# Kernel tuning notes

Measured on AMD Instinct MI355X. Metric: run time of the kernel, lower is better.

Reference implementation:

```python
import jax, jax.numpy as jnp
import numpy as np

E, N, D_IN, D_EMB, H = 4096, 4096, 256, 64, 8
HD = D_EMB * H
N_ETYPES, N_NTYPES = 4, 2
SCALE = D_EMB ** 0.5
EPS = 1e-5


def _layernorm(x, g, b):
    mu = jnp.mean(x, axis=-1, keepdims=True)
    var = jnp.var(x, axis=-1, keepdims=True)
    return (x - mu) / jnp.sqrt(var + EPS) * g + b


def setup_inputs() -> dict:
    key = jax.random.key(0)
    ks = jax.random.split(key, 14)
    s_in = 1.0 / np.sqrt(D_IN)
    s_cat = 1.0 / np.sqrt(HD + D_IN)
    return {
        "hyperedge_features": jax.random.normal(ks[0], (E, D_IN), jnp.float32),
        "node_features": jax.random.normal(ks[1], (N, D_IN), jnp.float32),
        "incidence_matrix": jax.random.randint(ks[2], (N, E), 0, 2, jnp.int32),
        "node_types": jax.random.randint(ks[3], (N,), 0, N_NTYPES, jnp.int32),
        "hyperedge_types": jax.random.randint(ks[4], (E,), 0, N_ETYPES, jnp.int32),
        # per-type expert weights (no bias in torch Linears)
        "Wq": jax.random.uniform(ks[5], (N_ETYPES, D_IN, HD), jnp.float32, -s_in, s_in),
        "Wk": jax.random.uniform(ks[6], (N_NTYPES, D_IN, HD), jnp.float32, -s_in, s_in),
        "Wv": jax.random.uniform(ks[7], (N_NTYPES, D_IN, HD), jnp.float32, -s_in, s_in),
        "Wo": jax.random.uniform(ks[8], (HD + D_IN, D_IN), jnp.float32, -s_cat, s_cat),
        "bo": jax.random.uniform(ks[9], (D_IN,), jnp.float32, -s_cat, s_cat),
        "gamma_e": jnp.ones((D_IN,), jnp.float32),
        "beta_e": jnp.zeros((D_IN,), jnp.float32),
        "gamma_n": jnp.ones((D_IN,), jnp.float32),
        "beta_n": jnp.zeros((D_IN,), jnp.float32),
    }


def reference(hyperedge_features, node_features, incidence_matrix, node_types,
              hyperedge_types, Wq, Wk, Wv, Wo, bo, gamma_e, beta_e, gamma_n, beta_n):
    he = _layernorm(hyperedge_features, gamma_e, beta_e)   # [E, D_IN]
    nf = _layernorm(node_features, gamma_n, beta_n)        # [N, D_IN]

    # type-conditional projections: compute all experts, gather per row
    q = jnp.einsum('ed,tdk->tek', he, Wq)[hyperedge_types, jnp.arange(E)]  # [E, HD]
    k = jnp.einsum('nd,tdk->tnk', nf, Wk)[node_types, jnp.arange(N)]      # [N, HD]
    v = jnp.einsum('nd,tdk->tnk', nf, Wv)[node_types, jnp.arange(N)]      # [N, HD]

    q = q.reshape(E, H, D_EMB).transpose(1, 0, 2)  # [H, E, D]
    k = k.reshape(N, H, D_EMB).transpose(1, 0, 2)  # [H, N, D]
    v = v.reshape(N, H, D_EMB).transpose(1, 0, 2)  # [H, N, D]

    scores = jnp.einsum('hed,hnd->hen', q, k) / SCALE        # [H, E, N]
    mask = incidence_matrix.T[None]                           # [1, E, N]
    scores = jnp.where(mask == 0, -jnp.inf, scores)
    weights = jax.nn.softmax(scores, axis=-1)                 # dropout in eval mode => identity

    out = jnp.einsum('hen,hnd->hed', weights, v)              # [H, E, D]
    out = out.transpose(1, 0, 2).reshape(E, HD)               # [E, HD]
    out = jax.nn.silu(out)

    final = jnp.concatenate([he, out], axis=-1) @ Wo + bo     # [E, D_IN]
    return final, scores
```

## Files before the change

kernel.cpp:

```cpp
#include <hip/hip_runtime.h>
#include <math.h>

#define E 4096
#define NN 4096
#define DIN 256
#define DEMB 64
#define NH 8
#define HD 512
#define EPS 1e-5f

typedef __bf16 bf16x8 __attribute__((ext_vector_type(8)));
typedef float f32x4 __attribute__((ext_vector_type(4)));

union FRS { uint4 u; bf16x8 b; unsigned short s[8]; };
union H4  { ushort4 u; unsigned short s[4]; };

#define MFMA __builtin_amdgcn_mfma_f32_16x16x32_bf16

__device__ __forceinline__ void splitf(float f, unsigned short& hs, unsigned short& ls) {
    unsigned u = __float_as_uint(f);
    hs = (unsigned short)(u >> 16);
    float rem = f - __uint_as_float(u & 0xffff0000u);
    ls = (unsigned short)(__float_as_uint(rem) >> 16);
}

__global__ void zero_counts(int* counts) {
    if (threadIdx.x < 8) counts[threadIdx.x] = 0;
}

__global__ void bucket_kernel(const int* __restrict__ et, const int* __restrict__ nt,
                              int* counts, int* ie, int* in_) {
    int i = blockIdx.x * 256 + threadIdx.x;
    if (i < E) {
        int t = et[i];
        int p = atomicAdd(&counts[t], 1);
        ie[t * E + p] = i;
    } else {
        int j = i - E;
        int t = nt[j];
        int p = atomicAdd(&counts[4 + t], 1);
        in_[t * NN + p] = j;
    }
}

__global__ __launch_bounds__(256) void incbits_kernel(const int* __restrict__ inc,
                                                      unsigned long long* __restrict__ ib) {
    int n = blockIdx.x;
    int l = threadIdx.x & 63, w = threadIdx.x >> 6;
    const int* row = inc + (size_t)n * E;
#pragma unroll
    for (int i = 0; i < 16; i++) {
        int word = i * 4 + w;
        unsigned long long b = __ballot(row[word * 64 + l] != 0);
        if (l == 0) ib[(size_t)n * 64 + word] = b;
    }
}

__global__ void bit_transpose(const unsigned long long* __restrict__ ib,
                              unsigned long long* __restrict__ it) {
    int nw = blockIdx.x, ew = blockIdx.y;
    int j = threadIdx.x;
    unsigned long long wv = ib[(size_t)(nw * 64 + j) * 64 + ew];
    unsigned long long mine = 0;
    for (int t2 = 0; t2 < 64; t2++) {
        unsigned long long b = __ballot((int)((wv >> t2) & 1ull));
        if (t2 == j) mine = b;
    }
    it[(size_t)(ew * 64 + j) * 64 + nw] = mine;
}

__device__ __forceinline__ float block_reduce_sum(float v, float* sm) {
    __syncthreads();
#pragma unroll
    for (int o = 32; o > 0; o >>= 1) v += __shfl_down(v, o, 64);
    int w = threadIdx.x >> 6, lane = threadIdx.x & 63;
    if (lane == 0) sm[w] = v;
    __syncthreads();
    return sm[0] + sm[1] + sm[2] + sm[3];
}

__global__ __launch_bounds__(256) void ln_kernel(const float* __restrict__ ef, const float* __restrict__ nf_in,
                          const float* __restrict__ ge, const float* __restrict__ be,
                          const float* __restrict__ gn, const float* __restrict__ bn,
                          float* __restrict__ he, float* __restrict__ nfo) {
    int row = blockIdx.x;
    const float* src; float* dst; const float* g; const float* b;
    if (row < E) { src = ef + (size_t)row * DIN; dst = he + (size_t)row * DIN; g = ge; b = be; }
    else { int r = row - E; src = nf_in + (size_t)r * DIN; dst = nfo + (size_t)r * DIN; g = gn; b = bn; }
    __shared__ float sm[4];
    int t = threadIdx.x;
    float x = src[t];
    float mu = block_reduce_sum(x, sm) * (1.f / DIN);
    float d = x - mu;
    float var = block_reduce_sum(d * d, sm) * (1.f / DIN);
    float rstd = rsqrtf(var + EPS);
    dst[t] = d * rstd * g[t] + b[t];
}

__global__ __launch_bounds__(256) void wconv(const float* __restrict__ src,
        char* __restrict__ dst, int Ktot, int Ctot) {
    int cb = blockIdx.x, kb = blockIdx.y, z = blockIdx.z;
    int CB = Ctot >> 6, KB = Ktot >> 6;
    const float* S = src + (size_t)z * Ktot * Ctot + (size_t)(kb * 64) * Ctot + cb * 64;
    char* D = dst + (((size_t)((z * CB + cb) * KB + kb)) << 14);
    __shared__ float Ls[64][68];
    int tid = threadIdx.x;
    int k = tid >> 2, cq = (tid & 3) * 16;
#pragma unroll
    for (int j = 0; j < 4; j++)
        *(float4*)&Ls[k][cq + j * 4] = *(const float4*)&S[(size_t)k * Ctot + cq + j * 4];
    __syncthreads();
    int c = tid >> 2, kq = (tid & 3) * 16;
    int sw = (c & 7) << 4;
#pragma unroll
    for (int grp = 0; grp < 4; grp++) {
        int k0 = kq + grp * 4;
        H4 hi, lo;
#pragma unroll
        for (int i = 0; i < 4; i++) splitf(Ls[k0 + i][c], hi.s[i], lo.s[i]);
        int off = (c * 128 + k0 * 2) ^ sw;
        *(ushort4*)(D + off) = hi.u;
        *(ushort4*)(D + 8192 + off) = lo.u;
    }
}

__global__ __launch_bounds__(256) void proj_mfma(const float* __restrict__ X,
        const char* __restrict__ wimg, const int* __restrict__ idx,
        const int* __restrict__ counts, int idxStride, int matBase,
        float* __restrict__ out) {
    int t = blockIdx.z;
    int cnt = counts[t];
    int r0 = blockIdx.y * 64;
    if (r0 >= cnt) return;
    int cb = blockIdx.x;
    const int* ib = idx + (size_t)t * idxStride;
    int tid = threadIdx.x;
    int w = tid >> 6, l = tid & 63, g = l >> 4, q = l & 15;
    __shared__ __align__(16) char XW[32768];
    int sm = tid >> 2, skq = (tid & 3) * 16;
    int srow = (r0 + sm < cnt) ? ib[r0 + sm] : -1;
    const int swz = (q & 7) << 4;
    const int sswz = (sm & 7) << 4;
    f32x4 acc[4] = {};
    const char* wtb = wimg + (((size_t)((matBase + t) * 8 + cb) * 4) << 14);
    for (int kb = 0; kb < 4; kb++) {
        __syncthreads();
#pragma unroll
        for (int c4 = 0; c4 < 4; c4++) {
            int gk = kb * 64 + skq + c4 * 4;
            float4 xv = (srow >= 0) ? *(const float4*)&X[(size_t)srow * DIN + gk]
                                    : make_float4(0.f, 0.f, 0.f, 0.f);
            float xf[4] = {xv.x, xv.y, xv.z, xv.w};
            H4 hi, lo;
#pragma unroll
            for (int i = 0; i < 4; i++) splitf(xf[i], hi.s[i], lo.s[i]);
            int off = (sm * 128 + (skq + c4 * 4) * 2) ^ sswz;
            *(ushort4*)(XW + off) = hi.u;
            *(ushort4*)(XW + 8192 + off) = lo.u;
        }
        const char* wt = wtb + ((size_t)kb << 14);
#pragma unroll
        for (int i = 0; i < 4; i++)
            *(uint4*)(XW + 16384 + i * 4096 + tid * 16) = *(const uint4*)(wt + i * 4096 + tid * 16);
        __syncthreads();
        FRS bh[2], bl[2];
#pragma unroll
        for (int ks = 0; ks < 2; ks++) {
            int boff = (w * 16 + q) * 128 + ((ks * 64 + g * 16) ^ swz);
            bh[ks].u = *(const uint4*)(XW + 16384 + boff);
            bl[ks].u = *(const uint4*)(XW + 24576 + boff);
        }
#pragma unroll
        for (int mt = 0; mt < 4; mt++) {
#pragma unroll
            for (int ks = 0; ks < 2; ks++) {
                int aoff = (mt * 16 + q) * 128 + ((ks * 64 + g * 16) ^ swz);
                FRS ah, al;
                ah.u = *(const uint4*)(XW + aoff);
                al.u = *(const uint4*)(XW + 8192 + aoff);
                acc[mt] = MFMA(ah.b, bh[ks].b, acc[mt], 0, 0, 0);
                acc[mt] = MFMA(ah.b, bl[ks].b, acc[mt], 0, 0, 0);
                acc[mt] = MFMA(al.b, bh[ks].b, acc[mt], 0, 0, 0);
            }
        }
    }
#pragma unroll
    for (int mt = 0; mt < 4; mt++)
#pragma unroll
        for (int r = 0; r < 4; r++) {
            int rg = r0 + mt * 16 + 4 * g + r;
            if (rg < cnt)
                out[(size_t)ib[rg] * HD + cb * 64 + w * 16 + q] = acc[mt][r];
        }
}

__global__ __launch_bounds__(256) void kconv(const float* __restrict__ kbuf,
                                             char* __restrict__ stage) {
    int gid = blockIdx.x * 256 + threadIdx.x;
    int d8 = gid & 7, hh = (gid >> 3) & 7;
    int n = gid >> 6;
    const float* src = kbuf + (size_t)n * HD + hh * 64 + d8 * 8;
    float4 a = *(const float4*)src, b = *(const float4*)(src + 4);
    float fv[8] = {a.x, a.y, a.z, a.w, b.x, b.y, b.z, b.w};
    FRS hi, lo;
#pragma unroll
    for (int j = 0; j < 8; j++) splitf(fv[j], hi.s[j], lo.s[j]);
    char* blk = stage + ((size_t)(hh * 64 + (n >> 6)) << 15);
    int nl = n & 63;
    int off = (nl * 128 + d8 * 16) ^ ((nl & 7) << 4);
    *(uint4*)(blk + off) = hi.u;
    *(uint4*)(blk + 8192 + off) = lo.u;
}

__global__ __launch_bounds__(256) void vconv(const float* __restrict__ vbuf,
                                             char* __restrict__ stage) {
    int tt = blockIdx.x, hh = blockIdx.y;
    __shared__ float Ls[64][68];
    int tid = threadIdx.x;
    int n = tid >> 2, q4 = (tid & 3) * 16;
#pragma unroll
    for (int j = 0; j < 4; j++)
        *(float4*)&Ls[n][q4 + j * 4] =
            *(const float4*)&vbuf[(size_t)(tt * 64 + n) * HD + hh * DEMB + q4 + j * 4];
    __syncthreads();
    char* blk = stage + ((size_t)(hh * 64 + tt) << 15);
    int d = tid >> 2, ng = tid & 3;
    int dsw = (d & 7) << 4;
#pragma unroll
    for (int sub = 0; sub < 4; sub++) {
        int n0 = ng * 16 + sub * 4;
        H4 hi, lo;
#pragma unroll
        for (int i = 0; i < 4; i++) splitf(Ls[n0 + i][d], hi.s[i], lo.s[i]);
        int s0 = ((n0 >> 5) << 5) + (((n0 >> 2) & 3) << 3) + (((n0 >> 4) & 1) << 2);
        int off = (d * 128 + s0 * 2) ^ dsw;
        *(ushort4*)(blk + 16384 + off) = hi.u;
        *(ushort4*)(blk + 24576 + off) = lo.u;
    }
}

__global__ __launch_bounds__(256, 2) void attn_mfma(
    const float* __restrict__ qb, const char* __restrict__ kvstage,
    const unsigned long long* __restrict__ incT,
    float* __restrict__ sc, float* __restrict__ pO,
    float* __restrict__ pm, float* __restrict__ plv)
{
    const int bx = blockIdx.x, h = blockIdx.y, nz = blockIdx.z;
    const int tid = threadIdx.x;
    const int w = tid >> 6, l = tid & 63;
    const int g = l >> 4, q = l & 15;
    const int e_wave = bx * 128 + w * 32;
    const int T0 = nz * 32;

    __shared__ __align__(16) char kv[2][32768];

    FRS qh[2][2], ql[2][2];
#pragma unroll
    for (int et = 0; et < 2; et++) {
        const float* qrow = qb + (size_t)(e_wave + et * 16 + q) * HD + h * DEMB;
#pragma unroll
        for (int ks = 0; ks < 2; ks++) {
            float4 A = *(const float4*)(qrow + ks * 32 + g * 8);
            float4 B = *(const float4*)(qrow + ks * 32 + g * 8 + 4);
            float fv[8] = {A.x, A.y, A.z, A.w, B.x, B.y, B.z, B.w};
            FRS hh, ll;
#pragma unroll
            for (int j = 0; j < 8; j++) splitf(fv[j], hh.s[j], ll.s[j]);
            qh[et][ks] = hh; ql[et][ks] = ll;
        }
    }

    uint4 streg[8];
    {
        const char* gs = kvstage + ((size_t)(h * 64 + T0) << 15);
#pragma unroll
        for (int i = 0; i < 8; i++) streg[i] = *(const uint4*)(gs + i * 4096 + tid * 16);
#pragma unroll
        for (int i = 0; i < 8; i++) *(uint4*)(&kv[0][i * 4096 + tid * 16]) = streg[i];
    }
    __syncthreads();

    f32x4 oacc[2][4];
#pragma unroll
    for (int et = 0; et < 2; et++)
#pragma unroll
        for (int dt = 0; dt < 4; dt++) oacc[et][dt] = (f32x4){0.f, 0.f, 0.f, 0.f};
    float mrow[2] = {-INFINITY, -INFINITY}, lrow[2] = {0.f, 0.f};
    const int swz = (q & 7) << 4;

    for (int tt = 0; tt < 32; tt++) {
        const int t = T0 + tt;
        const int cur = tt & 1;
        if (tt < 31) {
            const char* gs = kvstage + ((size_t)(h * 64 + t + 1) << 15);
#pragma unroll
            for (int i = 0; i < 8; i++) streg[i] = *(const uint4*)(gs + i * 4096 + tid * 16);
        }
        f32x4 sacc[2][4];
#pragma unroll
        for (int et = 0; et < 2; et++)
#pragma unroll
            for (int nt = 0; nt < 4; nt++) sacc[et][nt] = (f32x4){0.f, 0.f, 0.f, 0.f};
        const char* Kh = &kv[cur][0];
        const char* Kl = &kv[cur][8192];
#pragma unroll
        for (int ks = 0; ks < 2; ks++) {
#pragma unroll
            for (int nt = 0; nt < 4; nt++) {
                int off = (nt * 16 + q) * 128 + ((ks * 64 + g * 16) ^ swz);
                FRS ah, al;
                ah.u = *(const uint4*)(Kh + off);
                al.u = *(const uint4*)(Kl + off);
#pragma unroll
                for (int et = 0; et < 2; et++) {
                    sacc[et][nt] = MFMA(ah.b, qh[et][ks].b, sacc[et][nt], 0, 0, 0);
                    sacc[et][nt] = MFMA(ah.b, ql[et][ks].b, sacc[et][nt], 0, 0, 0);
                    sacc[et][nt] = MFMA(al.b, qh[et][ks].b, sacc[et][nt], 0, 0, 0);
                }
            }
        }
        float alpha_s[2];
#pragma unroll
        for (int et = 0; et < 2; et++) {
            int e = e_wave + et * 16 + q;
            unsigned long long mw = incT[(size_t)e * 64 + t];
            float rmax = -INFINITY;
#pragma unroll
            for (int nt = 0; nt < 4; nt++) {
                unsigned nib = (unsigned)(mw >> (nt * 16 + g * 4)) & 0xfu;
                f32x4 s4 = sacc[et][nt];
                f32x4 w4;
#pragma unroll
                for (int r = 0; r < 4; r++) {
                    float v = s4[r] * 0.125f;
                    bool on = (nib >> r) & 1u;
                    w4[r] = on ? v : -1.0e30f;
                    s4[r] = on ? v : -INFINITY;
                    if (on) rmax = fmaxf(rmax, v);
                }
                __builtin_nontemporal_store(w4,
                    (f32x4*)(sc + ((size_t)h * E + e) * NN + (size_t)t * 64 + nt * 16 + g * 4));
                sacc[et][nt] = s4;
            }
            rmax = fmaxf(rmax, __shfl_xor(rmax, 16, 64));
            rmax = fmaxf(rmax, __shfl_xor(rmax, 32, 64));
            float mo = mrow[et];
            float mn = fmaxf(mo, rmax);
            float al = (mn == -INFINITY) ? 1.f : __expf(mo - mn);
            alpha_s[et] = al;
            mrow[et] = mn;
            float ls = 0.f;
#pragma unroll
            for (int nt = 0; nt < 4; nt++) {
                f32x4 s4 = sacc[et][nt];
#pragma unroll
                for (int r = 0; r < 4; r++) {
                    float p = (s4[r] == -INFINITY) ? 0.f : __expf(s4[r] - mn);
                    s4[r] = p; ls += p;
                }
                sacc[et][nt] = s4;
            }
            ls += __shfl_xor(ls, 16, 64);
            ls += __shfl_xor(ls, 32, 64);
            lrow[et] = lrow[et] * al + ls;
        }
#pragma unroll
        for (int et = 0; et < 2; et++)
#pragma unroll
            for (int dt = 0; dt < 4; dt++) oacc[et][dt] *= alpha_s[et];
        const char* Vh = &kv[cur][16384];
        const char* Vl = &kv[cur][24576];
#pragma unroll
        for (int ns = 0; ns < 2; ns++) {
            FRS pah[2], pal[2];
#pragma unroll
            for (int et = 0; et < 2; et++) {
                FRS ph, pl2;
#pragma unroll
                for (int w2 = 0; w2 < 4; w2++) {
                    int nt = 2 * ns + (w2 >> 1);
                    int rb = 2 * (w2 & 1);
                    splitf(sacc[et][nt][rb],     ph.s[2 * w2],     pl2.s[2 * w2]);
                    splitf(sacc[et][nt][rb + 1], ph.s[2 * w2 + 1], pl2.s[2 * w2 + 1]);
                }
                pah[et] = ph; pal[et] = pl2;
            }
#pragma unroll
            for (int dt = 0; dt < 4; dt++) {
                int off = (dt * 16 + q) * 128 + ((ns * 64 + g * 16) ^ swz);
                FRS vh, vl;
                vh.u = *(const uint4*)(Vh + off);
                vl.u = *(const uint4*)(Vl + off);
#pragma unroll
                for (int et = 0; et < 2; et++) {
                    oacc[et][dt] = MFMA(vh.b, pah[et].b, oacc[et][dt], 0, 0, 0);
                    oacc[et][dt] = MFMA(vh.b, pal[et].b, oacc[et][dt], 0, 0, 0);
                    oacc[et][dt] = MFMA(vl.b, pah[et].b, oacc[et][dt], 0, 0, 0);
                }
            }
        }
        if (tt < 31) {
#pragma unroll
            for (int i = 0; i < 8; i++) *(uint4*)(&kv[cur ^ 1][i * 4096 + tid * 16]) = streg[i];
        }
        __syncthreads();
    }
#pragma unroll
    for (int et = 0; et < 2; et++) {
        int e = e_wave + et * 16 + q;
        size_t base = (((size_t)h * E + e) * 2 + nz) * 64;
#pragma unroll
        for (int dt = 0; dt < 4; dt++) {
            *(float4*)&pO[base + dt * 16 + g * 4] =
                make_float4(oacc[et][dt][0], oacc[et][dt][1], oacc[et][dt][2], oacc[et][dt][3]);
        }
        if (g == 0) {
            pm[((size_t)h * E + e) * 2 + nz] = mrow[et];
            plv[((size_t)h * E + e) * 2 + nz] = lrow[et];
        }
    }
}

__global__ __launch_bounds__(256) void combine_kernel(const float* __restrict__ pO,
        const float* __restrict__ pm, const float* __restrict__ plv,
        float* __restrict__ ao) {
    int gid = blockIdx.x * 256 + threadIdx.x;
    int eh = gid >> 2, dq = (gid & 3) * 16;
    float m0 = pm[(size_t)eh * 2], m1 = pm[(size_t)eh * 2 + 1];
    float l0 = plv[(size_t)eh * 2], l1 = plv[(size_t)eh * 2 + 1];
    float m = fmaxf(m0, m1);
    float w0 = (m0 == -INFINITY) ? 0.f : __expf(m0 - m);
    float w1 = (m1 == -INFINITY) ? 0.f : __expf(m1 - m);
    float den = w0 * l0 + w1 * l1;
    float rinv = den > 0.f ? 1.f / den : 0.f;
    int h = eh >> 12, e = eh & 4095;
    const float* o0 = pO + (size_t)eh * 128;
    const float* o1 = o0 + 64;
    float* dst = ao + (size_t)e * HD + h * DEMB + dq;
#pragma unroll
    for (int j = 0; j < 4; j++) {
        float4 a = *(const float4*)(o0 + dq + j * 4);
        float4 b = *(const float4*)(o1 + dq + j * 4);
        *(float4*)(dst + j * 4) = make_float4(
            (w0 * a.x + w1 * b.x) * rinv, (w0 * a.y + w1 * b.y) * rinv,
            (w0 * a.z + w1 * b.z) * rinv, (w0 * a.w + w1 * b.w) * rinv);
    }
}

__global__ __launch_bounds__(256) void final_mfma(const float* __restrict__ he,
        const float* __restrict__ ao, const char* __restrict__ woimg,
        const float* __restrict__ bo, float* __restrict__ out) {
    int cb = blockIdx.x, rb = blockIdx.y;
    int tid = threadIdx.x;
    int w = tid >> 6, l = tid & 63, g = l >> 4, q = l & 15;
    __shared__ __align__(16) char XW[32768];
    int sm = tid >> 2, skq = (tid & 3) * 16;
    int grow = rb * 64 + sm;
    const int swz = (q & 7) << 4;
    const int sswz = (sm & 7) << 4;
    f32x4 acc[4] = {};
    for (int kb = 0; kb < 12; kb++) {
        __syncthreads();
#pragma unroll
        for (int c4 = 0; c4 < 4; c4++) {
            int gk = kb * 64 + skq + c4 * 4;
            float4 xv;
            if (gk < DIN) {
                xv = *(const float4*)&he[(size_t)grow * DIN + gk];
            } else {
                xv = *(const float4*)&ao[(size_t)grow * HD + gk - DIN];
                xv.x = xv.x / (1.f + __expf(-xv.x));
                xv.y = xv.y / (1.f + __expf(-xv.y));
                xv.z = xv.z / (1.f + __expf(-xv.z));
                xv.w = xv.w / (1.f + __expf(-xv.w));
            }
            float xf[4] = {xv.x, xv.y, xv.z, xv.w};
            H4 hi, lo;
#pragma unroll
            for (int i = 0; i < 4; i++) splitf(xf[i], hi.s[i], lo.s[i]);
            int off = (sm * 128 + (skq + c4 * 4) * 2) ^ sswz;
            *(ushort4*)(XW + off) = hi.u;
            *(ushort4*)(XW + 8192 + off) = lo.u;
        }
        const char* wt = woimg + (((size_t)(cb * 12 + kb)) << 14);
#pragma unroll
        for (int i = 0; i < 4; i++)
            *(uint4*)(XW + 16384 + i * 4096 + tid * 16) = *(const uint4*)(wt + i * 4096 + tid * 16);
        __syncthreads();
        FRS bh[2], bl[2];
#pragma unroll
        for (int ks = 0; ks < 2; ks++) {
            int boff = (w * 16 + q) * 128 + ((ks * 64 + g * 16) ^ swz);
            bh[ks].u = *(const uint4*)(XW + 16384 + boff);
            bl[ks].u = *(const uint4*)(XW + 24576 + boff);
        }
#pragma unroll
        for (int mt = 0; mt < 4; mt++) {
#pragma unroll
            for (int ks = 0; ks < 2; ks++) {
                int aoff = (mt * 16 + q) * 128 + ((ks * 64 + g * 16) ^ swz);
                FRS ah, al;
                ah.u = *(const uint4*)(XW + aoff);
                al.u = *(const uint4*)(XW + 8192 + aoff);
                acc[mt] = MFMA(ah.b, bh[ks].b, acc[mt], 0, 0, 0);
                acc[mt] = MFMA(ah.b, bl[ks].b, acc[mt], 0, 0, 0);
                acc[mt] = MFMA(al.b, bh[ks].b, acc[mt], 0, 0, 0);
            }
        }
    }
    float bv = bo[cb * 64 + w * 16 + q];
#pragma unroll
    for (int mt = 0; mt < 4; mt++)
#pragma unroll
        for (int r = 0; r < 4; r++) {
            out[(size_t)(rb * 64 + mt * 16 + 4 * g + r) * DIN + cb * 64 + w * 16 + q] =
                acc[mt][r] + bv;
        }
}

extern "C" void kernel_launch(void* const* d_in, const int* in_sizes, int n_in,
                              void* d_out, int out_size, void* d_ws, size_t ws_size,
                              hipStream_t stream) {
    const float* ef     = (const float*)d_in[0];
    const float* nfeat  = (const float*)d_in[1];
    const int*   inc    = (const int*)d_in[2];
    const int*   ntypes = (const int*)d_in[3];
    const int*   etypes = (const int*)d_in[4];
    const float* Wq     = (const float*)d_in[5];
    const float* Wk     = (const float*)d_in[6];
    const float* Wv     = (const float*)d_in[7];
    const float* Wo     = (const float*)d_in[8];
    const float* bo     = (const float*)d_in[9];
    const float* ge     = (const float*)d_in[10];
    const float* be     = (const float*)d_in[11];
    const float* gn     = (const float*)d_in[12];
    const float* bn     = (const float*)d_in[13];

    float* out = (float*)d_out;
    float* sc  = out + (size_t)E * DIN;

    float* ws  = (float*)d_ws;
    float* he  = ws;
    float* nfo = ws + 1048576;
    float* qb  = ws + 2097152;
    float* kb  = ws + 4194304;
    float* vb  = ws + 6291456;
    float* ao  = ws + 8388608;
    int* counts = (int*)(ws + 10485760);
    int* idx_e  = counts + 8;
    int* idx_n  = idx_e + 4 * E;
    char* kvstage = (char*)(ws + 10510848);
    unsigned long long* incb = (unsigned long long*)(ws + 14705152);
    unsigned long long* incT = (unsigned long long*)(ws + 15229440);
    char* wimg  = (char*)(ws + 15753728);
    char* woimg = (char*)(ws + 16802304);
    float* pO   = kb;
    float* pm   = ws + 16998912;
    float* plv  = ws + 17064448;

    zero_counts<<<1, 64, 0, stream>>>(counts);
    bucket_kernel<<<(E + NN) / 256, 256, 0, stream>>>(etypes, ntypes, counts, idx_e, idx_n);
    incbits_kernel<<<NN, 256, 0, stream>>>(inc, incb);
    bit_transpose<<<dim3(64, 64), 64, 0, stream>>>(incb, incT);
    ln_kernel<<<E + NN, 256, 0, stream>>>(ef, nfeat, ge, be, gn, bn, he, nfo);
    wconv<<<dim3(8, 4, 4), 256, 0, stream>>>(Wq, wimg, DIN, HD);
    wconv<<<dim3(8, 4, 2), 256, 0, stream>>>(Wk, wimg + (size_t)4 * 524288, DIN, HD);
    wconv<<<dim3(8, 4, 2), 256, 0, stream>>>(Wv, wimg + (size_t)6 * 524288, DIN, HD);
    wconv<<<dim3(4, 12, 1), 256, 0, stream>>>(Wo, woimg, DIN + HD, DIN);
    proj_mfma<<<dim3(8, 64, 4), 256, 0, stream>>>(he, wimg, idx_e, counts, E, 0, qb);
    proj_mfma<<<dim3(8, 64, 2), 256, 0, stream>>>(nfo, wimg, idx_n, counts + 4, NN, 4, kb);
    proj_mfma<<<dim3(8, 64, 2), 256, 0, stream>>>(nfo, wimg, idx_n, counts + 4, NN, 6, vb);
    kconv<<<1024, 256, 0, stream>>>(kb, kvstage);
    vconv<<<dim3(64, 8), 256, 0, stream>>>(vb, kvstage);
    attn_mfma<<<dim3(32, 8, 2), 256, 0, stream>>>(qb, kvstage, incT, sc, pO, pm, plv);
    combine_kernel<<<512, 256, 0, stream>>>(pO, pm, plv, ao);
    final_mfma<<<dim3(4, 64), 256, 0, stream>>>(he, ao, woimg, bo, out);
}
```

Measured before the change: 948.0 us.

## Merge launches, use warp-per-row layernorm, fold combine into final GEMM

Merges the three weight-conversion launches into one, the three projection launches into one, and the K and V staging kernels into one. Layernorm now uses one wavefront per row with float4 loads and shuffle reductions instead of block-wide shared-memory reductions. The split-softmax combine step moves into the final GEMM's load phase, which removes the intermediate attention-output buffer and one launch. The attention grid is flattened with the head index in the low bits, which changes block scheduling order.

```diff
diff --git a/kernel.cpp b/kernel.cpp
--- a/kernel.cpp
+++ b/kernel.cpp
@@ -69,40 +69,33 @@
     it[(size_t)(ew * 64 + j) * 64 + nw] = mine;
 }
 
-__device__ __forceinline__ float block_reduce_sum(float v, float* sm) {
-    __syncthreads();
-#pragma unroll
-    for (int o = 32; o > 0; o >>= 1) v += __shfl_down(v, o, 64);
-    int w = threadIdx.x >> 6, lane = threadIdx.x & 63;
-    if (lane == 0) sm[w] = v;
-    __syncthreads();
-    return sm[0] + sm[1] + sm[2] + sm[3];
-}
-
 __global__ __launch_bounds__(256) void ln_kernel(const float* __restrict__ ef, const float* __restrict__ nf_in,
                           const float* __restrict__ ge, const float* __restrict__ be,
                           const float* __restrict__ gn, const float* __restrict__ bn,
                           float* __restrict__ he, float* __restrict__ nfo) {
-    int row = blockIdx.x;
+    int w = threadIdx.x >> 6, l = threadIdx.x & 63;
+    int row = blockIdx.x * 4 + w;
     const float* src; float* dst; const float* g; const float* b;
     if (row < E) { src = ef + (size_t)row * DIN; dst = he + (size_t)row * DIN; g = ge; b = be; }
     else { int r = row - E; src = nf_in + (size_t)r * DIN; dst = nfo + (size_t)r * DIN; g = gn; b = bn; }
-    __shared__ float sm[4];
-    int t = threadIdx.x;
-    float x = src[t];
-    float mu = block_reduce_sum(x, sm) * (1.f / DIN);
-    float d = x - mu;
-    float var = block_reduce_sum(d * d, sm) * (1.f / DIN);
-    float rstd = rsqrtf(var + EPS);
-    dst[t] = d * rstd * g[t] + b[t];
-}
-
-__global__ __launch_bounds__(256) void wconv(const float* __restrict__ src,
-        char* __restrict__ dst, int Ktot, int Ctot) {
-    int cb = blockIdx.x, kb = blockIdx.y, z = blockIdx.z;
-    int CB = Ctot >> 6, KB = Ktot >> 6;
-    const float* S = src + (size_t)z * Ktot * Ctot + (size_t)(kb * 64) * Ctot + cb * 64;
-    char* D = dst + (((size_t)((z * CB + cb) * KB + kb)) << 14);
+    float4 x = *(const float4*)&src[l * 4];
+    float s = x.x + x.y + x.z + x.w;
+#pragma unroll
+    for (int o = 32; o > 0; o >>= 1) s += __shfl_xor(s, o, 64);
+    float mu = s * (1.f / DIN);
+    float4 d = make_float4(x.x - mu, x.y - mu, x.z - mu, x.w - mu);
+    float v = d.x * d.x + d.y * d.y + d.z * d.z + d.w * d.w;
+#pragma unroll
+    for (int o = 32; o > 0; o >>= 1) v += __shfl_xor(v, o, 64);
+    float rstd = rsqrtf(v * (1.f / DIN) + EPS);
+    float4 gg = *(const float4*)&g[l * 4];
+    float4 bb = *(const float4*)&b[l * 4];
+    *(float4*)&dst[l * 4] = make_float4(d.x * rstd * gg.x + bb.x, d.y * rstd * gg.y + bb.y,
+                                        d.z * rstd * gg.z + bb.z, d.w * rstd * gg.w + bb.w);
+}
+
+__device__ __forceinline__ void wconv_body(const float* __restrict__ S, char* __restrict__ D,
+                                           int Ctot) {
     __shared__ float Ls[64][68];
     int tid = threadIdx.x;
     int k = tid >> 2, cq = (tid & 3) * 16;
@@ -124,16 +117,45 @@
     }
 }
 
-__global__ __launch_bounds__(256) void proj_mfma(const float* __restrict__ X,
-        const char* __restrict__ wimg, const int* __restrict__ idx,
-        const int* __restrict__ counts, int idxStride, int matBase,
-        float* __restrict__ out) {
-    int t = blockIdx.z;
-    int cnt = counts[t];
+__global__ __launch_bounds__(256) void wconv(const float* __restrict__ src,
+        char* __restrict__ dst, int Ktot, int Ctot) {
+    int cb = blockIdx.x, kb = blockIdx.y;
+    int CB = Ctot >> 6, KB = Ktot >> 6;
+    const float* S = src + (size_t)(kb * 64) * Ctot + cb * 64;
+    char* D = dst + (((size_t)(cb * KB + kb)) << 14);
+    (void)CB;
+    wconv_body(S, D, Ctot);
+}
+
+__global__ __launch_bounds__(256) void wconv_qkv(const float* __restrict__ Wq,
+        const float* __restrict__ Wk, const float* __restrict__ Wv,
+        char* __restrict__ dst) {
+    int cb = blockIdx.x, kb = blockIdx.y, z = blockIdx.z;
+    const float* S;
+    if (z < 4) S = Wq + (size_t)z * DIN * HD;
+    else if (z < 6) S = Wk + (size_t)(z - 4) * DIN * HD;
+    else S = Wv + (size_t)(z - 6) * DIN * HD;
+    S += (size_t)(kb * 64) * HD + cb * 64;
+    char* D = dst + (((size_t)((z * 8 + cb) * 4 + kb)) << 14);
+    wconv_body(S, D, HD);
+}
+
+__global__ __launch_bounds__(256) void proj_all(const float* __restrict__ Xe,
+        const float* __restrict__ Xn, const char* __restrict__ wimg,
+        const int* __restrict__ idx_e, const int* __restrict__ idx_n,
+        const int* __restrict__ counts,
+        float* __restrict__ qb, float* __restrict__ kbuf, float* __restrict__ vbuf) {
+    int z = blockIdx.z;
+    const float* X; const int* ib; int cnt; float* out;
+    if (z < 4) { X = Xe; ib = idx_e + (size_t)z * E; cnt = counts[z]; out = qb; }
+    else {
+        int tt = (z - 4) & 1;
+        X = Xn; ib = idx_n + (size_t)tt * NN; cnt = counts[4 + tt];
+        out = (z < 6) ? kbuf : vbuf;
+    }
     int r0 = blockIdx.y * 64;
     if (r0 >= cnt) return;
     int cb = blockIdx.x;
-    const int* ib = idx + (size_t)t * idxStride;
     int tid = threadIdx.x;
     int w = tid >> 6, l = tid & 63, g = l >> 4, q = l & 15;
     __shared__ __align__(16) char XW[32768];
@@ -142,7 +164,7 @@
     const int swz = (q & 7) << 4;
     const int sswz = (sm & 7) << 4;
     f32x4 acc[4] = {};
-    const char* wtb = wimg + (((size_t)((matBase + t) * 8 + cb) * 4) << 14);
+    const char* wtb = wimg + (((size_t)(z * 8 + cb) * 4) << 14);
     for (int kb = 0; kb < 4; kb++) {
         __syncthreads();
 #pragma unroll
@@ -194,48 +216,50 @@
         }
 }
 
-__global__ __launch_bounds__(256) void kconv(const float* __restrict__ kbuf,
-                                             char* __restrict__ stage) {
-    int gid = blockIdx.x * 256 + threadIdx.x;
-    int d8 = gid & 7, hh = (gid >> 3) & 7;
-    int n = gid >> 6;
-    const float* src = kbuf + (size_t)n * HD + hh * 64 + d8 * 8;
-    float4 a = *(const float4*)src, b = *(const float4*)(src + 4);
-    float fv[8] = {a.x, a.y, a.z, a.w, b.x, b.y, b.z, b.w};
-    FRS hi, lo;
-#pragma unroll
-    for (int j = 0; j < 8; j++) splitf(fv[j], hi.s[j], lo.s[j]);
-    char* blk = stage + ((size_t)(hh * 64 + (n >> 6)) << 15);
-    int nl = n & 63;
-    int off = (nl * 128 + d8 * 16) ^ ((nl & 7) << 4);
-    *(uint4*)(blk + off) = hi.u;
-    *(uint4*)(blk + 8192 + off) = lo.u;
-}
-
-__global__ __launch_bounds__(256) void vconv(const float* __restrict__ vbuf,
-                                             char* __restrict__ stage) {
-    int tt = blockIdx.x, hh = blockIdx.y;
+__global__ __launch_bounds__(256) void kvconv(const float* __restrict__ kbuf,
+                                              const float* __restrict__ vbuf,
+                                              char* __restrict__ stage) {
     __shared__ float Ls[64][68];
-    int tid = threadIdx.x;
-    int n = tid >> 2, q4 = (tid & 3) * 16;
-#pragma unroll
-    for (int j = 0; j < 4; j++)
-        *(float4*)&Ls[n][q4 + j * 4] =
-            *(const float4*)&vbuf[(size_t)(tt * 64 + n) * HD + hh * DEMB + q4 + j * 4];
-    __syncthreads();
-    char* blk = stage + ((size_t)(hh * 64 + tt) << 15);
-    int d = tid >> 2, ng = tid & 3;
-    int dsw = (d & 7) << 4;
-#pragma unroll
-    for (int sub = 0; sub < 4; sub++) {
-        int n0 = ng * 16 + sub * 4;
-        H4 hi, lo;
-#pragma unroll
-        for (int i = 0; i < 4; i++) splitf(Ls[n0 + i][d], hi.s[i], lo.s[i]);
-        int s0 = ((n0 >> 5) << 5) + (((n0 >> 2) & 3) << 3) + (((n0 >> 4) & 1) << 2);
-        int off = (d * 128 + s0 * 2) ^ dsw;
-        *(ushort4*)(blk + 16384 + off) = hi.u;
-        *(ushort4*)(blk + 24576 + off) = lo.u;
+    int bidx = blockIdx.x;
+    if (bidx < 1024) {
+        int gid = bidx * 256 + threadIdx.x;
+        int d8 = gid & 7, hh = (gid >> 3) & 7;
+        int n = gid >> 6;
+        const float* src = kbuf + (size_t)n * HD + hh * 64 + d8 * 8;
+        float4 a = *(const float4*)src, b = *(const float4*)(src + 4);
+        float fv[8] = {a.x, a.y, a.z, a.w, b.x, b.y, b.z, b.w};
+        FRS hi, lo;
+#pragma unroll
+        for (int j = 0; j < 8; j++) splitf(fv[j], hi.s[j], lo.s[j]);
+        char* blk = stage + ((size_t)(hh * 64 + (n >> 6)) << 15);
+        int nl = n & 63;
+        int off = (nl * 128 + d8 * 16) ^ ((nl & 7) << 4);
+        *(uint4*)(blk + off) = hi.u;
+        *(uint4*)(blk + 8192 + off) = lo.u;
+    } else {
+        int idx = bidx - 1024;
+        int tt = idx & 63, hh = idx >> 6;
+        int tid = threadIdx.x;
+        int n = tid >> 2, q4 = (tid & 3) * 16;
+#pragma unroll
+        for (int j = 0; j < 4; j++)
+            *(float4*)&Ls[n][q4 + j * 4] =
+                *(const float4*)&vbuf[(size_t)(tt * 64 + n) * HD + hh * DEMB + q4 + j * 4];
+        __syncthreads();
+        char* blk = stage + ((size_t)(hh * 64 + tt) << 15);
+        int d = tid >> 2, ng = tid & 3;
+        int dsw = (d & 7) << 4;
+#pragma unroll
+        for (int sub = 0; sub < 4; sub++) {
+            int n0 = ng * 16 + sub * 4;
+            H4 hi, lo;
+#pragma unroll
+            for (int i = 0; i < 4; i++) splitf(Ls[n0 + i][d], hi.s[i], lo.s[i]);
+            int s0 = ((n0 >> 5) << 5) + (((n0 >> 2) & 3) << 3) + (((n0 >> 4) & 1) << 2);
+            int off = (d * 128 + s0 * 2) ^ dsw;
+            *(ushort4*)(blk + 16384 + off) = hi.u;
+            *(ushort4*)(blk + 24576 + off) = lo.u;
+        }
     }
 }
 
@@ -245,7 +269,10 @@
     float* __restrict__ sc, float* __restrict__ pO,
     float* __restrict__ pm, float* __restrict__ plv)
 {
-    const int bx = blockIdx.x, h = blockIdx.y, nz = blockIdx.z;
+    const int flat = blockIdx.x;
+    const int h = flat & 7;
+    const int bx = (flat >> 3) & 31;
+    const int nz = flat >> 8;
     const int tid = threadIdx.x;
     const int w = tid >> 6, l = tid & 63;
     const int g = l >> 4, q = l & 15;
@@ -421,34 +448,9 @@
     }
 }
 
-__global__ __launch_bounds__(256) void combine_kernel(const float* __restrict__ pO,
-        const float* __restrict__ pm, const float* __restrict__ plv,
-        float* __restrict__ ao) {
-    int gid = blockIdx.x * 256 + threadIdx.x;
-    int eh = gid >> 2, dq = (gid & 3) * 16;
-    float m0 = pm[(size_t)eh * 2], m1 = pm[(size_t)eh * 2 + 1];
-    float l0 = plv[(size_t)eh * 2], l1 = plv[(size_t)eh * 2 + 1];
-    float m = fmaxf(m0, m1);
-    float w0 = (m0 == -INFINITY) ? 0.f : __expf(m0 - m);
-    float w1 = (m1 == -INFINITY) ? 0.f : __expf(m1 - m);
-    float den = w0 * l0 + w1 * l1;
-    float rinv = den > 0.f ? 1.f / den : 0.f;
-    int h = eh >> 12, e = eh & 4095;
-    const float* o0 = pO + (size_t)eh * 128;
-    const float* o1 = o0 + 64;
-    float* dst = ao + (size_t)e * HD + h * DEMB + dq;
-#pragma unroll
-    for (int j = 0; j < 4; j++) {
-        float4 a = *(const float4*)(o0 + dq + j * 4);
-        float4 b = *(const float4*)(o1 + dq + j * 4);
-        *(float4*)(dst + j * 4) = make_float4(
-            (w0 * a.x + w1 * b.x) * rinv, (w0 * a.y + w1 * b.y) * rinv,
-            (w0 * a.z + w1 * b.z) * rinv, (w0 * a.w + w1 * b.w) * rinv);
-    }
-}
-
 __global__ __launch_bounds__(256) void final_mfma(const float* __restrict__ he,
-        const float* __restrict__ ao, const char* __restrict__ woimg,
+        const float* __restrict__ pO, const float* __restrict__ pm,
+        const float* __restrict__ plv, const char* __restrict__ woimg,
         const float* __restrict__ bo, float* __restrict__ out) {
     int cb = blockIdx.x, rb = blockIdx.y;
     int tid = threadIdx.x;
@@ -461,14 +463,34 @@
     f32x4 acc[4] = {};
     for (int kb = 0; kb < 12; kb++) {
         __syncthreads();
+        float w0 = 0.f, w1 = 0.f, rinv = 0.f;
+        const float* o0 = nullptr;
+        if (kb >= 4) {
+            int hh = kb - 4;
+            size_t eh = (size_t)hh * E + grow;
+            float m0 = pm[eh * 2], m1 = pm[eh * 2 + 1];
+            float l0 = plv[eh * 2], l1 = plv[eh * 2 + 1];
+            float mx = fmaxf(m0, m1);
+            w0 = (m0 == -INFINITY) ? 0.f : __expf(m0 - mx);
+            w1 = (m1 == -INFINITY) ? 0.f : __expf(m1 - mx);
+            float den = w0 * l0 + w1 * l1;
+            rinv = den > 0.f ? 1.f / den : 0.f;
+            o0 = pO + eh * 128;
+        }
 #pragma unroll
         for (int c4 = 0; c4 < 4; c4++) {
-            int gk = kb * 64 + skq + c4 * 4;
             float4 xv;
-            if (gk < DIN) {
+            if (kb < 4) {
+                int gk = kb * 64 + skq + c4 * 4;
                 xv = *(const float4*)&he[(size_t)grow * DIN + gk];
             } else {
-                xv = *(const float4*)&ao[(size_t)grow * HD + gk - DIN];
+                int dq = skq + c4 * 4;
+                float4 a = *(const float4*)(o0 + dq);
+                float4 b = *(const float4*)(o0 + 64 + dq);
+                xv.x = (w0 * a.x + w1 * b.x) * rinv;
+                xv.y = (w0 * a.y + w1 * b.y) * rinv;
+                xv.z = (w0 * a.z + w1 * b.z) * rinv;
+                xv.w = (w0 * a.w + w1 * b.w) * rinv;
                 xv.x = xv.x / (1.f + __expf(-xv.x));
                 xv.y = xv.y / (1.f + __expf(-xv.y));
                 xv.z = xv.z / (1.f + __expf(-xv.z));
@@ -545,7 +567,6 @@
     float* qb  = ws + 2097152;
     float* kb  = ws + 4194304;
     float* vb  = ws + 6291456;
-    float* ao  = ws + 8388608;
     int* counts = (int*)(ws + 10485760);
     int* idx_e  = counts + 8;
     int* idx_n  = idx_e + 4 * E;
@@ -562,17 +583,11 @@
     bucket_kernel<<<(E + NN) / 256, 256, 0, stream>>>(etypes, ntypes, counts, idx_e, idx_n);
     incbits_kernel<<<NN, 256, 0, stream>>>(inc, incb);
     bit_transpose<<<dim3(64, 64), 64, 0, stream>>>(incb, incT);
-    ln_kernel<<<E + NN, 256, 0, stream>>>(ef, nfeat, ge, be, gn, bn, he, nfo);
-    wconv<<<dim3(8, 4, 4), 256, 0, stream>>>(Wq, wimg, DIN, HD);
-    wconv<<<dim3(8, 4, 2), 256, 0, stream>>>(Wk, wimg + (size_t)4 * 524288, DIN, HD);
-    wconv<<<dim3(8, 4, 2), 256, 0, stream>>>(Wv, wimg + (size_t)6 * 524288, DIN, HD);
-    wconv<<<dim3(4, 12, 1), 256, 0, stream>>>(Wo, woimg, DIN + HD, DIN);
-    proj_mfma<<<dim3(8, 64, 4), 256, 0, stream>>>(he, wimg, idx_e, counts, E, 0, qb);
-    proj_mfma<<<dim3(8, 64, 2), 256, 0, stream>>>(nfo, wimg, idx_n, counts + 4, NN, 4, kb);
-    proj_mfma<<<dim3(8, 64, 2), 256, 0, stream>>>(nfo, wimg, idx_n, counts + 4, NN, 6, vb);
-    kconv<<<1024, 256, 0, stream>>>(kb, kvstage);
-    vconv<<<dim3(64, 8), 256, 0, stream>>>(vb, kvstage);
-    attn_mfma<<<dim3(32, 8, 2), 256, 0, stream>>>(qb, kvstage, incT, sc, pO, pm, plv);
-    combine_kernel<<<512, 256, 0, stream>>>(pO, pm, plv, ao);
-    final_mfma<<<dim3(4, 64), 256, 0, stream>>>(he, ao, woimg, bo, out);
-}
+    ln_kernel<<<(E + NN) / 4, 256, 0, stream>>>(ef, nfeat, ge, be, gn, bn, he, nfo);
+    wconv_qkv<<<dim3(8, 4, 8), 256, 0, stream>>>(Wq, Wk, Wv, wimg);
+    wconv<<<dim3(4, 12), 256, 0, stream>>>(Wo, woimg, DIN + HD, DIN);
+    proj_all<<<dim3(8, 64, 8), 256, 0, stream>>>(he, nfo, wimg, idx_e, idx_n, counts, qb, kb, vb);
+    kvconv<<<1536, 256, 0, stream>>>(kb, vb, kvstage);
+    attn_mfma<<<512, 256, 0, stream>>>(qb, kvstage, incT, sc, pO, pm, plv);
+    final_mfma<<<dim3(4, 64), 256, 0, stream>>>(he, pO, pm, plv, woimg, bo, out);
+}
```

Result: faster. 923.2 us (-2.6%).
